# Kernel tuning notes

Measured on AMD Instinct MI355X. Metric: run time of the kernel, lower is better.

The kernel has to match this reference:

```python
import jax, jax.numpy as jnp
import numpy as np

B, N, F, H, OUT = 64, 512, 128, 256, 6


def setup_inputs() -> dict:
    key = jax.random.key(0)
    ks = jax.random.split(key, 20)
    s = 0.02
    inp = {
        "x": jax.random.normal(ks[0], (B * N, F), dtype=jnp.float32),
        "edge_index": jax.random.randint(ks[1], (2, 16), 0, B * N),
        "edge_weight": jax.random.uniform(ks[2], (16,), dtype=jnp.float32),
        "batch": jnp.repeat(jnp.arange(B, dtype=jnp.int64), N),
        "sigma": jax.random.uniform(ks[3], (1,), dtype=jnp.float32),
        "Wg": s * jax.random.normal(ks[4], (F, F)), "bg": jnp.zeros((F,)),
        "Wrel0": s * jax.random.normal(ks[5], (F, H)), "Wroot0": s * jax.random.normal(ks[6], (F, H)), "brel0": jnp.zeros((H,)),
        "Wrel1": s * jax.random.normal(ks[7], (H, H)), "Wroot1": s * jax.random.normal(ks[8], (H, H)), "brel1": jnp.zeros((H,)),
        "Wrel2": s * jax.random.normal(ks[9], (H, H)), "Wroot2": s * jax.random.normal(ks[10], (H, H)), "brel2": jnp.zeros((H,)),
        "W1": s * jax.random.normal(ks[11], (H, H)), "b1": jnp.zeros((H,)),
        "Wout": s * jax.random.normal(ks[12], (H, OUT)), "bout": jnp.zeros((OUT,)),
    }
    return inp


def _forward(x, sigma, Wg, bg, Wrel0, Wroot0, brel0, Wrel1, Wroot1, brel1,
             Wrel2, Wroot2, brel2, W1, b1, Wout, bout):
    # gdmLinear
    h = x @ Wg + bg                      # [B*N, F]
    hw = h.reshape(B, N, -1)             # to_dense_batch (equal-size windows)
    # pairwise squared distances per window -> Gaussian kernel
    sq = jnp.sum(hw * hw, axis=-1)       # [B, N]
    dist = jnp.maximum(sq[:, :, None] + sq[:, None, :]
                       - 2.0 * jnp.einsum('bnf,bmf->bnm', hw, hw), 0.0)
    A = jnp.exp(-dist / (2.0 * sigma[0] ** 2))   # [B, N, N], all > 0
    A = A * (1.0 - jnp.eye(N, dtype=A.dtype))    # nonzero extraction drops self-loops

    def conv(h, Wrel, Wroot, brel):
        # GraphConv: out_i = W_rel @ sum_j A[j,i] * h_j + b_rel + W_root @ h_i
        agg = jnp.einsum('bji,bjf->bif', A, h)
        return agg @ Wrel + brel + h @ Wroot

    h = hw
    h = jax.nn.relu(conv(h, Wrel0, Wroot0, brel0))
    h = jax.nn.relu(conv(h, Wrel1, Wroot1, brel1))
    h = conv(h, Wrel2, Wroot2, brel2)
    g = jnp.mean(h, axis=1)              # global_mean_pool (equal-size graphs)
    g = jax.nn.relu(g @ W1 + b1)
    return g @ Wout + bout               # [B, OUT]


def reference(x, edge_index, edge_weight, batch, sigma, Wg, bg,
              Wrel0, Wroot0, brel0, Wrel1, Wroot1, brel1,
              Wrel2, Wroot2, brel2, W1, b1, Wout, bout):
    # edge_index / edge_weight / batch inputs are recomputed internally by GdmGNN
    return _forward(x, sigma, Wg, bg, Wrel0, Wroot0, brel0, Wrel1, Wroot1, brel1,
                    Wrel2, Wroot2, brel2, W1, b1, Wout, bout)
```

## Files before the change

### kernel.cpp

```cpp
#include <hip/hip_runtime.h>
#include <math.h>

#define Bsz 64
#define Nn 512
#define Ff 128
#define Hh 256
#define OUTD 6
#define MTOT (Bsz * Nn)

typedef __bf16 bf16x8 __attribute__((ext_vector_type(8)));
typedef float f32x4 __attribute__((ext_vector_type(4)));
typedef int int4v __attribute__((ext_vector_type(4)));
typedef unsigned short ushort4v __attribute__((ext_vector_type(4)));

__device__ __forceinline__ unsigned short f2bf(float f) {
    unsigned u = __float_as_uint(f);
    u += 0x7FFFu + ((u >> 16) & 1u);
    return (unsigned short)(u >> 16);
}
__device__ __forceinline__ float bf2f(unsigned short s) {
    return __uint_as_float(((unsigned)s) << 16);
}

#define SWZ(r) (((r) ^ ((r) >> 2)) & 3)

__device__ __forceinline__ void async_ld16(const unsigned short* g, unsigned short* l) {
    __builtin_amdgcn_global_load_lds(
        (const __attribute__((address_space(1))) void*)g,
        (__attribute__((address_space(3))) void*)l,
        16, 0, 0);
}

__device__ __forceinline__ void wait_vm(int n) {
    switch (n) {
        case 0: asm volatile("s_waitcnt vmcnt(0)" ::: "memory"); break;
        case 1: asm volatile("s_waitcnt vmcnt(1)" ::: "memory"); break;
        case 2: asm volatile("s_waitcnt vmcnt(2)" ::: "memory"); break;
        case 3: asm volatile("s_waitcnt vmcnt(3)" ::: "memory"); break;
        case 4: asm volatile("s_waitcnt vmcnt(4)" ::: "memory"); break;
        case 5: asm volatile("s_waitcnt vmcnt(5)" ::: "memory"); break;
        default: asm volatile("s_waitcnt vmcnt(6)" ::: "memory"); break;
    }
}
__device__ __forceinline__ void pipe_barrier(int n) {
    wait_vm(n);
    __builtin_amdgcn_s_barrier();
    __builtin_amdgcn_sched_barrier(0);
}

#define LDH 40
#define TSZ (128 * 32)
#define ATS (256 * 32)
#define AGP 136
#define AGP1 264

__global__ __launch_bounds__(512) void fused_l0(
    const unsigned short* __restrict__ h0T,
    const unsigned short* __restrict__ Arows,
    const unsigned short* __restrict__ h0b,
    const unsigned short* __restrict__ WrelT0,
    const unsigned short* __restrict__ WrootT0,
    const float* __restrict__ brel0,
    unsigned short* __restrict__ h1b,
    unsigned short* __restrict__ h1T)
{
    int id = blockIdx.x;
    int b = id & 63;
    int nt = id >> 6;
    int n0g = nt * 128;
    long nodeBase = (long)b * Nn + n0g;

    const unsigned short* HT = h0T + (long)b * Ff * Nn;
    const unsigned short* AR = Arows + (long)b * Nn * Nn;

    __shared__ unsigned short SA[3 * ATS];
    __shared__ unsigned short SB[3 * TSZ];
    __shared__ unsigned short aggL[128 * AGP];

    int tid = threadIdx.x;
    int lane = tid & 63;
    int wave = tid >> 6;
    int quad = lane >> 4, l16 = lane & 15;
    int sr = lane >> 2, sc = lane & 3;

    {
        int wm = (wave >> 1) * 32, wn = (wave & 1) * 64;
        f32x4 acc[2][4] = {};
        auto issue = [&](int g) {
            int kk = g << 5;
            unsigned short* Ad = SA + (g % 3) * ATS;
            unsigned short* Bd = SB + (g % 3) * TSZ;
            int r = wave * 16 + sr;
            int c = sc ^ SWZ(r);
            async_ld16(HT + (long)r * Nn + kk + c * 8, Ad + (wave * 16) * 32);
            async_ld16(AR + (long)(n0g + r) * Nn + kk + c * 8, Bd + (wave * 16) * 32);
        };
        issue(0); issue(1);
        for (int g = 0; g < 16; ++g) {
            pipe_barrier(g + 1 < 16 ? 2 : 0);
            if (g + 2 < 16) issue(g + 2);
            const unsigned short* Ab = SA + (g % 3) * ATS;
            const unsigned short* Bb = SB + (g % 3) * TSZ;
            bf16x8 af[2], bfr[4];
            #pragma unroll
            for (int i = 0; i < 2; ++i) {
                int r = wm + i * 16 + l16;
                af[i] = *(const bf16x8*)&Ab[r * 32 + (quad ^ SWZ(r)) * 8];
            }
            #pragma unroll
            for (int j = 0; j < 4; ++j) {
                int r = wn + j * 16 + l16;
                bfr[j] = *(const bf16x8*)&Bb[r * 32 + (quad ^ SWZ(r)) * 8];
            }
            #pragma unroll
            for (int i = 0; i < 2; ++i)
                #pragma unroll
                for (int j = 0; j < 4; ++j)
                    acc[i][j] = __builtin_amdgcn_mfma_f32_16x16x32_bf16(
                        af[i], bfr[j], acc[i][j], 0, 0, 0);
        }
        #pragma unroll
        for (int i = 0; i < 2; ++i) {
            int f = wm + i * 16 + quad * 4;
            #pragma unroll
            for (int j = 0; j < 4; ++j) {
                int nl = wn + j * 16 + l16;
                f32x4 v = acc[i][j];
                ushort4v p;
                p[0] = f2bf(v[0]); p[1] = f2bf(v[1]);
                p[2] = f2bf(v[2]); p[3] = f2bf(v[3]);
                *(ushort4v*)&aggL[nl * AGP + f] = p;
            }
        }
    }
    __syncthreads();

    {
        int wm = (wave >> 1) * 64, wn = (wave & 1) * 64;
        f32x4 acc[4][4] = {};
        auto issue2 = [&](int g) {
            const unsigned short* Wp = (g < 4) ? WrelT0 : WrootT0;
            int kk = (g & 3) << 5;
            unsigned short* Ad = SA + (g % 3) * ATS;
            int r = wave * 16 + sr;
            int c = sc ^ SWZ(r);
            async_ld16(Wp + (long)r * Ff + kk + c * 8, Ad + (wave * 16) * 32);
            int r2 = 128 + r;
            int c2 = sc ^ SWZ(r2);
            async_ld16(Wp + (long)r2 * Ff + kk + c2 * 8, Ad + (128 + wave * 16) * 32);
            if (g >= 4) {
                unsigned short* Bd = SB + (g % 3) * TSZ;
                async_ld16(h0b + (nodeBase + r) * Ff + kk + c * 8,
                           Bd + (wave * 16) * 32);
            }
        };
        issue2(0); issue2(1);
        for (int g = 0; g < 8; ++g) {
            int nx = g + 1;
            pipe_barrier(nx >= 8 ? 0 : (nx < 4 ? 2 : 3));
            if (g + 2 < 8) issue2(g + 2);
            const unsigned short* Ab = SA + (g % 3) * ATS;
            bf16x8 af[4], bfr[4];
            #pragma unroll
            for (int i = 0; i < 4; ++i) {
                int r = wm + i * 16 + l16;
                af[i] = *(const bf16x8*)&Ab[r * 32 + (quad ^ SWZ(r)) * 8];
            }
            if (g < 4) {
                #pragma unroll
                for (int j = 0; j < 4; ++j) {
                    int nl = wn + j * 16 + l16;
                    bfr[j] = *(const bf16x8*)&aggL[nl * AGP + (g << 5) + quad * 8];
                }
            } else {
                const unsigned short* Bb = SB + (g % 3) * TSZ;
                #pragma unroll
                for (int j = 0; j < 4; ++j) {
                    int r = wn + j * 16 + l16;
                    bfr[j] = *(const bf16x8*)&Bb[r * 32 + (quad ^ SWZ(r)) * 8];
                }
            }
            #pragma unroll
            for (int i = 0; i < 4; ++i)
                #pragma unroll
                for (int j = 0; j < 4; ++j)
                    acc[i][j] = __builtin_amdgcn_mfma_f32_16x16x32_bf16(
                        af[i], bfr[j], acc[i][j], 0, 0, 0);
        }
        #pragma unroll
        for (int i = 0; i < 4; ++i) {
            int of = wm + i * 16 + quad * 4;
            float b0 = brel0[of + 0], b1 = brel0[of + 1];
            float b2 = brel0[of + 2], b3 = brel0[of + 3];
            #pragma unroll
            for (int j = 0; j < 4; ++j) {
                int nl = wn + j * 16 + l16;
                f32x4 v = acc[i][j];
                float o0 = fmaxf(v[0] + b0, 0.f), o1 = fmaxf(v[1] + b1, 0.f);
                float o2 = fmaxf(v[2] + b2, 0.f), o3 = fmaxf(v[3] + b3, 0.f);
                ushort4v p;
                p[0] = f2bf(o0); p[1] = f2bf(o1); p[2] = f2bf(o2); p[3] = f2bf(o3);
                *(ushort4v*)&h1b[(nodeBase + nl) * Hh + of] = p;
                long base = ((long)b * Hh) * 512 + n0g + nl;
                h1T[base + (long)(of + 0) * 512] = p[0];
                h1T[base + (long)(of + 1) * 512] = p[1];
                h1T[base + (long)(of + 2) * 512] = p[2];
                h1T[base + (long)(of + 3) * 512] = p[3];
            }
        }
    }
}

__global__ __launch_bounds__(512) void fused_l1(
    const unsigned short* __restrict__ h1T,
    const unsigned short* __restrict__ Arows,
    const unsigned short* __restrict__ h1b,
    const unsigned short* __restrict__ WrelT1,
    const unsigned short* __restrict__ WrootT1,
    const float* __restrict__ brel1,
    const float* __restrict__ w,
    float* __restrict__ vpart, float* __restrict__ mpart)
{
    constexpr int BTS = 128 * 32;

    int id = blockIdx.x;
    int b = id & 63;
    int nt = id >> 6;
    int n0g = nt * 128;
    long nodeBase = (long)b * Nn + n0g;

    const unsigned short* HT = h1T + (long)b * Hh * Nn;
    const unsigned short* AR = Arows + (long)b * Nn * Nn;

    __shared__ unsigned short SA[3 * ATS];
    __shared__ unsigned short SB[3 * BTS];
    __shared__ unsigned short aggL[128 * AGP1];

    int tid = threadIdx.x;
    int lane = tid & 63;
    int wave = tid >> 6;
    int quad = lane >> 4, l16 = lane & 15;
    int wm = (wave >> 1) * 64;
    int wn = (wave & 1) * 64;
    int sr = lane >> 2, sc = lane & 3;

    {
        f32x4 acc[4][4] = {};
        auto issue = [&](int g) {
            int kk = g << 5;
            unsigned short* Ad = SA + (g % 3) * ATS;
            int r = wave * 16 + sr;
            int c = sc ^ SWZ(r);
            async_ld16(HT + (long)r * Nn + kk + c * 8, Ad + (wave * 16) * 32);
            int r2 = 128 + r;
            int c2 = sc ^ SWZ(r2);
            async_ld16(HT + (long)r2 * Nn + kk + c2 * 8, Ad + (128 + wave * 16) * 32);
            unsigned short* Bd = SB + (g % 3) * BTS;
            async_ld16(AR + (long)(n0g + r) * Nn + kk + c * 8, Bd + (wave * 16) * 32);
        };
        issue(0); issue(1);
        for (int g = 0; g < 16; ++g) {
            pipe_barrier(g + 1 < 16 ? 3 : 0);
            if (g + 2 < 16) issue(g + 2);
            const unsigned short* Ab = SA + (g % 3) * ATS;
            const unsigned short* Bb = SB + (g % 3) * BTS;
            bf16x8 af[4], bfr[4];
            #pragma unroll
            for (int i = 0; i < 4; ++i) {
                int r = wm + i * 16 + l16;
                af[i] = *(const bf16x8*)&Ab[r * 32 + (quad ^ SWZ(r)) * 8];
            }
            #pragma unroll
            for (int j = 0; j < 4; ++j) {
                int r = wn + j * 16 + l16;
                bfr[j] = *(const bf16x8*)&Bb[r * 32 + (quad ^ SWZ(r)) * 8];
            }
            #pragma unroll
            for (int i = 0; i < 4; ++i)
                #pragma unroll
                for (int j = 0; j < 4; ++j)
                    acc[i][j] = __builtin_amdgcn_mfma_f32_16x16x32_bf16(
                        af[i], bfr[j], acc[i][j], 0, 0, 0);
        }
        #pragma unroll
        for (int i = 0; i < 4; ++i) {
            int f = wm + i * 16 + quad * 4;
            #pragma unroll
            for (int j = 0; j < 4; ++j) {
                int nl = wn + j * 16 + l16;
                f32x4 v = acc[i][j];
                ushort4v p;
                p[0] = f2bf(v[0]); p[1] = f2bf(v[1]);
                p[2] = f2bf(v[2]); p[3] = f2bf(v[3]);
                *(ushort4v*)&aggL[nl * AGP1 + f] = p;
            }
        }
    }
    __syncthreads();

    f32x4 acc[4][4] = {};
    auto issue2 = [&](int g) {
        const unsigned short* Wp = (g < 8) ? WrelT1 : WrootT1;
        int kk = (g & 7) << 5;
        unsigned short* Ad = SA + (g % 3) * ATS;
        int r = wave * 16 + sr;
        int c = sc ^ SWZ(r);
        async_ld16(Wp + (long)r * Hh + kk + c * 8, Ad + (wave * 16) * 32);
        int r2 = 128 + r;
        int c2 = sc ^ SWZ(r2);
        async_ld16(Wp + (long)r2 * Hh + kk + c2 * 8, Ad + (128 + wave * 16) * 32);
        if (g >= 8) {
            unsigned short* Bd = SB + (g % 3) * BTS;
            async_ld16(h1b + (nodeBase + r) * Hh + kk + c * 8, Bd + (wave * 16) * 32);
        }
    };
    issue2(0); issue2(1);
    for (int g = 0; g < 16; ++g) {
        int nx = g + 1;
        pipe_barrier(nx >= 16 ? 0 : (nx < 8 ? 2 : 3));
        if (g + 2 < 16) issue2(g + 2);
        const unsigned short* Ab = SA + (g % 3) * ATS;
        bf16x8 af[4], bfr[4];
        #pragma unroll
        for (int i = 0; i < 4; ++i) {
            int r = wm + i * 16 + l16;
            af[i] = *(const bf16x8*)&Ab[r * 32 + (quad ^ SWZ(r)) * 8];
        }
        if (g < 8) {
            #pragma unroll
            for (int j = 0; j < 4; ++j) {
                int nl = wn + j * 16 + l16;
                bfr[j] = *(const bf16x8*)&aggL[nl * AGP1 + (g << 5) + quad * 8];
            }
        } else {
            const unsigned short* Bb = SB + (g % 3) * BTS;
            #pragma unroll
            for (int j = 0; j < 4; ++j) {
                int r = wn + j * 16 + l16;
                bfr[j] = *(const bf16x8*)&Bb[r * 32 + (quad ^ SWZ(r)) * 8];
            }
        }
        #pragma unroll
        for (int i = 0; i < 4; ++i)
            #pragma unroll
            for (int j = 0; j < 4; ++j)
                acc[i][j] = __builtin_amdgcn_mfma_f32_16x16x32_bf16(
                    af[i], bfr[j], acc[i][j], 0, 0, 0);
    }

    #pragma unroll
    for (int i = 0; i < 4; ++i) {
        int lf = wm + i * 16 + quad * 4;
        float b0 = brel1[lf + 0], b1 = brel1[lf + 1];
        float b2 = brel1[lf + 2], b3 = brel1[lf + 3];
        float vp0 = 0.f, vp1 = 0.f, vp2 = 0.f, vp3 = 0.f;
        float mp0 = 0.f, mp1 = 0.f, mp2 = 0.f, mp3 = 0.f;
        #pragma unroll
        for (int j = 0; j < 4; ++j) {
            long node = nodeBase + wn + j * 16 + l16;
            f32x4 v = acc[i][j];
            float o0 = fmaxf(v[0] + b0, 0.f), o1 = fmaxf(v[1] + b1, 0.f);
            float o2 = fmaxf(v[2] + b2, 0.f), o3 = fmaxf(v[3] + b3, 0.f);
            float h0v = bf2f(f2bf(o0)), h1v = bf2f(f2bf(o1));
            float h2v = bf2f(f2bf(o2)), h3v = bf2f(f2bf(o3));
            float wv = w[node];
            vp0 += wv * h0v; vp1 += wv * h1v; vp2 += wv * h2v; vp3 += wv * h3v;
            mp0 += h0v; mp1 += h1v; mp2 += h2v; mp3 += h3v;
        }
        #pragma unroll
        for (int m = 1; m < 16; m <<= 1) {
            vp0 += __shfl_xor(vp0, m); vp1 += __shfl_xor(vp1, m);
            vp2 += __shfl_xor(vp2, m); vp3 += __shfl_xor(vp3, m);
            mp0 += __shfl_xor(mp0, m); mp1 += __shfl_xor(mp1, m);
            mp2 += __shfl_xor(mp2, m); mp3 += __shfl_xor(mp3, m);
        }
        if (l16 == 0) {
            long o = ((long)(b * 8 + nt * 2 + (wave & 1))) * Hh + lf;
            float4 vv = {vp0, vp1, vp2, vp3};
            float4 mm = {mp0, mp1, mp2, mp3};
            *(float4*)&vpart[o] = vv;
            *(float4*)&mpart[o] = mm;
        }
    }
}

__global__ __launch_bounds__(256) void prep_h0(
    const float* __restrict__ x, const float* __restrict__ Wg,
    const float* __restrict__ bg,
    const float* __restrict__ Wrel0, const float* __restrict__ Wroot0,
    const float* __restrict__ Wrel1, const float* __restrict__ Wroot1,
    unsigned short* __restrict__ T0, unsigned short* __restrict__ T1,
    unsigned short* __restrict__ T2, unsigned short* __restrict__ T3,
    float* __restrict__ w,
    unsigned short* __restrict__ h0b, unsigned short* __restrict__ h0T,
    float* __restrict__ sqv)
{
    if (blockIdx.x < 896) {
        int idx = blockIdx.x * 256 + threadIdx.x;
        if (idx >= 196608) { w[idx - 196608] = 0.f; return; }
        const float* src; unsigned short* dst; int kin; int e;
        if      (idx <  32768) { src = Wrel0;  dst = T0; kin = 128; e = idx; }
        else if (idx <  65536) { src = Wroot0; dst = T1; kin = 128; e = idx - 32768; }
        else if (idx < 131072) { src = Wrel1;  dst = T2; kin = 256; e = idx - 65536; }
        else                   { src = Wroot1; dst = T3; kin = 256; e = idx - 131072; }
        int o = (kin == 128) ? (e >> 7) : (e >> 8);
        int i = e & (kin - 1);
        dst[e] = f2bf(src[(long)i * 256 + o]);
        return;
    }

    __shared__ unsigned short As[128 * LDH];
    __shared__ unsigned short Bs[128 * LDH];
    __shared__ float rsq[128];

    int tid = threadIdx.x;
    int lane = tid & 63;
    int wave = tid >> 6;
    int quad = lane >> 4, l16 = lane & 15;
    int wm = (wave >> 1) * 64, wn = (wave & 1) * 64;
    int m0 = (blockIdx.x - 896) * 128;

    f32x4 acc[4][4] = {};

    for (int k0 = 0; k0 < Ff; k0 += 32) {
        __syncthreads();
        #pragma unroll
        for (int l = 0; l < 2; ++l) {
            int idx = tid + l * 256;
            int r = idx >> 2, ch = idx & 3;
            const float* px = x + (long)(m0 + r) * Ff + k0 + ch * 8;
            float4 xa = *(const float4*)px;
            float4 xb = *(const float4*)(px + 4);
            ushort4v pa, pb;
            pa[0] = f2bf(xa.x); pa[1] = f2bf(xa.y); pa[2] = f2bf(xa.z); pa[3] = f2bf(xa.w);
            pb[0] = f2bf(xb.x); pb[1] = f2bf(xb.y); pb[2] = f2bf(xb.z); pb[3] = f2bf(xb.w);
            *(ushort4v*)&As[r * LDH + ch * 8] = pa;
            *(ushort4v*)&As[r * LDH + ch * 8 + 4] = pb;
            int kk = k0 + ch * 8;
            ushort4v qa, qb;
            #pragma unroll
            for (int u = 0; u < 4; ++u) qa[u] = f2bf(Wg[(long)(kk + u) * 128 + r]);
            #pragma unroll
            for (int u = 0; u < 4; ++u) qb[u] = f2bf(Wg[(long)(kk + 4 + u) * 128 + r]);
            *(ushort4v*)&Bs[r * LDH + ch * 8] = qa;
            *(ushort4v*)&Bs[r * LDH + ch * 8 + 4] = qb;
        }
        __syncthreads();
        bf16x8 af[4], bfr[4];
        #pragma unroll
        for (int i = 0; i < 4; ++i)
            af[i] = *(const bf16x8*)&As[(wm + i * 16 + l16) * LDH + quad * 8];
        #pragma unroll
        for (int j = 0; j < 4; ++j)
            bfr[j] = *(const bf16x8*)&Bs[(wn + j * 16 + l16) * LDH + quad * 8];
        #pragma unroll
        for (int i = 0; i < 4; ++i)
            #pragma unroll
            for (int j = 0; j < 4; ++j)
                acc[i][j] = __builtin_amdgcn_mfma_f32_16x16x32_bf16(
                    af[i], bfr[j], acc[i][j], 0, 0, 0);
    }

    if (tid < 128) rsq[tid] = 0.f;
    __syncthreads();

    #pragma unroll
    for (int i = 0; i < 4; ++i) {
        int lrow = wm + i * 16 + quad * 4;
        int mb = m0 + lrow;
        float rp0 = 0.f, rp1 = 0.f, rp2 = 0.f, rp3 = 0.f;
        #pragma unroll
        for (int j = 0; j < 4; ++j) {
            int n = wn + j * 16 + l16;
            f32x4 v = acc[i][j];
            float bv = bg[n];
            unsigned short s0 = f2bf(v[0] + bv), s1 = f2bf(v[1] + bv);
            unsigned short s2 = f2bf(v[2] + bv), s3 = f2bf(v[3] + bv);
            h0b[(long)(mb + 0) * Ff + n] = s0;
            h0b[(long)(mb + 1) * Ff + n] = s1;
            h0b[(long)(mb + 2) * Ff + n] = s2;
            h0b[(long)(mb + 3) * Ff + n] = s3;
            ushort4v p; p[0] = s0; p[1] = s1; p[2] = s2; p[3] = s3;
            long ti = ((long)(mb >> 9) * Ff + n) * 512 + (mb & 511);
            *(ushort4v*)&h0T[ti] = p;
            float f0 = bf2f(s0), f1 = bf2f(s1), f2 = bf2f(s2), f3 = bf2f(s3);
            rp0 += f0 * f0; rp1 += f1 * f1; rp2 += f2 * f2; rp3 += f3 * f3;
        }
        #pragma unroll
        for (int m = 1; m < 16; m <<= 1) {
            rp0 += __shfl_xor(rp0, m);
            rp1 += __shfl_xor(rp1, m);
            rp2 += __shfl_xor(rp2, m);
            rp3 += __shfl_xor(rp3, m);
        }
        if (l16 == 0) {
            atomicAdd(&rsq[lrow + 0], rp0);
            atomicAdd(&rsq[lrow + 1], rp1);
            atomicAdd(&rsq[lrow + 2], rp2);
            atomicAdd(&rsq[lrow + 3], rp3);
        }
    }
    __syncthreads();
    if (tid < 128) sqv[m0 + tid] = rsq[tid];
}

__global__ __launch_bounds__(512) void gram_A_mfma(
    const unsigned short* __restrict__ h0b, const float* __restrict__ sqv,
    const float* __restrict__ sigma, unsigned short* __restrict__ Aout,
    float* __restrict__ w)
{
    int id = blockIdx.x;
    int b = id & 63;
    int t = id >> 6;
    int i0 = (t & 3) * 128, j0 = (t >> 2) * 128;

    const unsigned short* H = h0b + (long)b * Nn * Ff;
    const float* SQ = sqv + (long)b * Nn;
    unsigned short* Ab = Aout + (long)b * Nn * Nn;

    __shared__ unsigned short Is[2 * TSZ];
    __shared__ unsigned short Js[2 * TSZ];
    __shared__ float rsum[128];

    int tid = threadIdx.x;
    int lane = tid & 63;
    int wave = tid >> 6;
    int quad = lane >> 4, l16 = lane & 15;
    int wm = (wave >> 1) * 32, wn = (wave & 1) * 64;

    int sr = lane >> 2, sc = lane & 3;

    f32x4 acc[2][4] = {};

    auto issue = [&](int g) {
        int kk = g << 5;
        unsigned short* Id = Is + (g & 1) * TSZ;
        unsigned short* Jd = Js + (g & 1) * TSZ;
        int r = wave * 16 + sr;
        int c = sc ^ SWZ(r);
        async_ld16(H + (long)(i0 + r) * Ff + kk + c * 8, Id + (wave * 16) * 32);
        async_ld16(H + (long)(j0 + r) * Ff + kk + c * 8, Jd + (wave * 16) * 32);
    };

    issue(0);
    for (int g = 0; g < (Ff >> 5); ++g) {
        __syncthreads();
        if (g + 1 < (Ff >> 5)) issue(g + 1);
        const unsigned short* Ib = Is + (g & 1) * TSZ;
        const unsigned short* Jb = Js + (g & 1) * TSZ;
        bf16x8 af[2], bfr[4];
        #pragma unroll
        for (int i = 0; i < 2; ++i) {
            int r = wm + i * 16 + l16;
            af[i] = *(const bf16x8*)&Ib[r * 32 + (quad ^ SWZ(r)) * 8];
        }
        #pragma unroll
        for (int j = 0; j < 4; ++j) {
            int r = wn + j * 16 + l16;
            bfr[j] = *(const bf16x8*)&Jb[r * 32 + (quad ^ SWZ(r)) * 8];
        }
        #pragma unroll
        for (int i = 0; i < 2; ++i)
            #pragma unroll
            for (int j = 0; j < 4; ++j)
                acc[i][j] = __builtin_amdgcn_mfma_f32_16x16x32_bf16(
                    af[i], bfr[j], acc[i][j], 0, 0, 0);
    }

    if (tid < 128) rsum[tid] = 0.f;
    __syncthreads();

    float s = sigma[0];
    float inv2s2 = 1.0f / (2.0f * s * s);
    #pragma unroll
    for (int i = 0; i < 2; ++i) {
        int lrow = wm + i * 16 + quad * 4;
        int rb = i0 + lrow;
        float rs0 = 0.f, rs1 = 0.f, rs2 = 0.f, rs3 = 0.f;
        #pragma unroll
        for (int j = 0; j < 4; ++j) {
            int c = j0 + wn + j * 16 + l16;
            float sqc = SQ[c];
            f32x4 v = acc[i][j];
            ushort4v pk;
            float av[4];
            #pragma unroll
            for (int r4 = 0; r4 < 4; ++r4) {
                int r = rb + r4;
                float d = fmaxf(SQ[r] + sqc - 2.0f * v[r4], 0.0f);
                unsigned short a = (r == c) ? (unsigned short)0
                                            : f2bf(__expf(-d * inv2s2));
                pk[r4] = a;
                av[r4] = bf2f(a);
            }
            *(ushort4v*)&Ab[(long)c * Nn + rb] = pk;
            rs0 += av[0]; rs1 += av[1]; rs2 += av[2]; rs3 += av[3];
        }
        #pragma unroll
        for (int m = 1; m < 16; m <<= 1) {
            rs0 += __shfl_xor(rs0, m);
            rs1 += __shfl_xor(rs1, m);
            rs2 += __shfl_xor(rs2, m);
            rs3 += __shfl_xor(rs3, m);
        }
        if (l16 == 0) {
            atomicAdd(&rsum[lrow + 0], rs0);
            atomicAdd(&rsum[lrow + 1], rs1);
            atomicAdd(&rsum[lrow + 2], rs2);
            atomicAdd(&rsum[lrow + 3], rs3);
        }
    }
    __syncthreads();
    if (tid < 128) atomicAdd(&w[(long)b * Nn + i0 + tid], rsum[tid]);
}

__global__ __launch_bounds__(256) void head_kernel(
    const float* __restrict__ vpart, const float* __restrict__ mpart,
    const float* __restrict__ Wrel2, const float* __restrict__ Wroot2,
    const float* __restrict__ brel2,
    const float* __restrict__ W1, const float* __restrict__ b1,
    const float* __restrict__ Wout, const float* __restrict__ bout,
    float* __restrict__ out)
{
    int b = blockIdx.x;
    int j = threadIdx.x;
    __shared__ float vs[Hh], ms[Hh], gs[Hh], g2[Hh];
    float vp = 0.f, mp = 0.f;
    #pragma unroll
    for (int p = 0; p < 8; ++p) {
        long o = ((long)(b * 8 + p)) * Hh + j;
        vp += vpart[o];
        mp += mpart[o];
    }
    vs[j] = vp * (1.0f / (float)Nn);
    ms[j] = mp * (1.0f / (float)Nn);
    __syncthreads();
    float s = brel2[j];
    for (int c = 0; c < Hh; ++c)
        s += vs[c] * Wrel2[c * Hh + j] + ms[c] * Wroot2[c * Hh + j];
    gs[j] = s;
    __syncthreads();
    float t = b1[j];
    for (int k = 0; k < Hh; ++k) t += gs[k] * W1[k * Hh + j];
    g2[j] = fmaxf(t, 0.f);
    __syncthreads();
    if (j < OUTD) {
        float s2 = bout[j];
        for (int k = 0; k < Hh; ++k) s2 += g2[k] * Wout[k * OUTD + j];
        out[b * OUTD + j] = s2;
    }
}

extern "C" void kernel_launch(void* const* d_in, const int* in_sizes, int n_in,
                              void* d_out, int out_size, void* d_ws, size_t ws_size,
                              hipStream_t stream) {
    const float* x      = (const float*)d_in[0];
    const float* sigma  = (const float*)d_in[4];
    const float* Wg     = (const float*)d_in[5];
    const float* bg     = (const float*)d_in[6];
    const float* Wrel0  = (const float*)d_in[7];
    const float* Wroot0 = (const float*)d_in[8];
    const float* brel0  = (const float*)d_in[9];
    const float* Wrel1  = (const float*)d_in[10];
    const float* Wroot1 = (const float*)d_in[11];
    const float* brel1  = (const float*)d_in[12];
    const float* Wrel2  = (const float*)d_in[13];
    const float* Wroot2 = (const float*)d_in[14];
    const float* brel2  = (const float*)d_in[15];
    const float* W1     = (const float*)d_in[16];
    const float* b1     = (const float*)d_in[17];
    const float* Wout   = (const float*)d_in[18];
    const float* bout   = (const float*)d_in[19];
    float* out = (float*)d_out;

    char* ws = (char*)d_ws;
    unsigned short* h0b  = (unsigned short*)(ws + 16777216);
    unsigned short* h0T  = (unsigned short*)(ws + 25165824);
    float*          sq   = (float*)(ws + 33554432);
    unsigned short* Aadj = (unsigned short*)(ws + 33685504);
    unsigned short* h1b  = (unsigned short*)(ws + 84017152);
    unsigned short* h1T  = (unsigned short*)(ws + 100794368);
    unsigned short* WrelT0  = (unsigned short*)(ws + 167903232);
    unsigned short* WrootT0 = (unsigned short*)(ws + 167968768);
    unsigned short* WrelT1  = (unsigned short*)(ws + 168034304);
    unsigned short* WrootT1 = (unsigned short*)(ws + 168165376);
    float*          w     = (float*)(ws + 168558592);
    float*          vpart = (float*)(ws + 168689664);
    float*          mpart = (float*)(ws + 169213952);

    prep_h0<<<1152, 256, 0, stream>>>(x, Wg, bg, Wrel0, Wroot0, Wrel1, Wroot1,
                                      WrelT0, WrootT0, WrelT1, WrootT1,
                                      w, h0b, h0T, sq);

    gram_A_mfma<<<dim3(16 * Bsz, 1, 1), 512, 0, stream>>>(h0b, sq, sigma, Aadj, w);

    fused_l0<<<dim3(4 * Bsz, 1, 1), 512, 0, stream>>>(
        h0T, Aadj, h0b, WrelT0, WrootT0, brel0, h1b, h1T);

    fused_l1<<<dim3(4 * Bsz, 1, 1), 512, 0, stream>>>(
        h1T, Aadj, h1b, WrelT1, WrootT1, brel1, w, vpart, mpart);

    head_kernel<<<Bsz, 256, 0, stream>>>(vpart, mpart, Wrel2, Wroot2, brel2,
                                         W1, b1, Wout, bout, out);
}
```

Measured before the change: 212.4 us.

## Exploit Gram matrix symmetry to compute only upper-triangular tiles

The Gaussian adjacency kernel now launches 10 tile-pairs per graph instead of 16, computing only the upper-triangular 128x128 blocks of the symmetric distance matrix. Each off-diagonal tile writes both its transposed layout directly and its mirror through an LDS-staged transpose, and accumulates row and column sums into the degree vector. This cuts MFMA and exp work by about a third, at the cost of extra LDS traffic and a second global store pass per tile.

```diff
diff --git a/kernel.cpp b/kernel.cpp
--- a/kernel.cpp
+++ b/kernel.cpp
@@ -10,7 +10,6 @@
 
 typedef __bf16 bf16x8 __attribute__((ext_vector_type(8)));
 typedef float f32x4 __attribute__((ext_vector_type(4)));
-typedef int int4v __attribute__((ext_vector_type(4)));
 typedef unsigned short ushort4v __attribute__((ext_vector_type(4)));
 
 __device__ __forceinline__ unsigned short f2bf(float f) {
@@ -53,6 +52,7 @@
 #define ATS (256 * 32)
 #define AGP 136
 #define AGP1 264
+#define ATP 132
 
 __global__ __launch_bounds__(512) void fused_l0(
     const unsigned short* __restrict__ h0T,
@@ -504,38 +504,46 @@
     if (tid < 128) sqv[m0 + tid] = rsq[tid];
 }
 
-__global__ __launch_bounds__(512) void gram_A_mfma(
+__global__ __launch_bounds__(512) void gram_A_sym(
     const unsigned short* __restrict__ h0b, const float* __restrict__ sqv,
     const float* __restrict__ sigma, unsigned short* __restrict__ Aout,
     float* __restrict__ w)
 {
     int id = blockIdx.x;
     int b = id & 63;
-    int t = id >> 6;
-    int i0 = (t & 3) * 128, j0 = (t >> 2) * 128;
+    int tp = id >> 6;
+    int ti, tj;
+    if      (tp < 4) { ti = 0; tj = tp; }
+    else if (tp < 7) { ti = 1; tj = tp - 3; }
+    else if (tp < 9) { ti = 2; tj = tp - 5; }
+    else             { ti = 3; tj = 3; }
+    int i0 = ti * 128, j0 = tj * 128;
+    bool offd = (ti != tj);
 
     const unsigned short* H = h0b + (long)b * Nn * Ff;
     const float* SQ = sqv + (long)b * Nn;
     unsigned short* Ab = Aout + (long)b * Nn * Nn;
 
-    __shared__ unsigned short Is[2 * TSZ];
-    __shared__ unsigned short Js[2 * TSZ];
-    __shared__ float rsum[128];
+    __shared__ unsigned short POOL[128 * ATP];
+    __shared__ float rsI[128];
+    __shared__ float rsJ[128];
 
     int tid = threadIdx.x;
     int lane = tid & 63;
     int wave = tid >> 6;
     int quad = lane >> 4, l16 = lane & 15;
     int wm = (wave >> 1) * 32, wn = (wave & 1) * 64;
-
     int sr = lane >> 2, sc = lane & 3;
+
+    unsigned short* Is = POOL;
+    unsigned short* Js = POOL + 8192;
 
     f32x4 acc[2][4] = {};
 
     auto issue = [&](int g) {
         int kk = g << 5;
-        unsigned short* Id = Is + (g & 1) * TSZ;
-        unsigned short* Jd = Js + (g & 1) * TSZ;
+        unsigned short* Id = Is + (g & 1) * 4096;
+        unsigned short* Jd = Js + (g & 1) * 4096;
         int r = wave * 16 + sr;
         int c = sc ^ SWZ(r);
         async_ld16(H + (long)(i0 + r) * Ff + kk + c * 8, Id + (wave * 16) * 32);
@@ -546,8 +554,8 @@
     for (int g = 0; g < (Ff >> 5); ++g) {
         __syncthreads();
         if (g + 1 < (Ff >> 5)) issue(g + 1);
-        const unsigned short* Ib = Is + (g & 1) * TSZ;
-        const unsigned short* Jb = Js + (g & 1) * TSZ;
+        const unsigned short* Ib = Is + (g & 1) * 4096;
+        const unsigned short* Jb = Js + (g & 1) * 4096;
         bf16x8 af[2], bfr[4];
         #pragma unroll
         for (int i = 0; i < 2; ++i) {
@@ -567,33 +575,44 @@
                     af[i], bfr[j], acc[i][j], 0, 0, 0);
     }
 
-    if (tid < 128) rsum[tid] = 0.f;
-    __syncthreads();
-
+    if (tid < 128) { rsI[tid] = 0.f; rsJ[tid] = 0.f; }
+    __syncthreads();
+
+    unsigned short* AT = POOL;
     float s = sigma[0];
     float inv2s2 = 1.0f / (2.0f * s * s);
+    float colsum0 = 0.f, colsum1 = 0.f, colsum2 = 0.f, colsum3 = 0.f;
+
     #pragma unroll
     for (int i = 0; i < 2; ++i) {
         int lrow = wm + i * 16 + quad * 4;
-        int rb = i0 + lrow;
+        int rbg = i0 + lrow;
         float rs0 = 0.f, rs1 = 0.f, rs2 = 0.f, rs3 = 0.f;
         #pragma unroll
         for (int j = 0; j < 4; ++j) {
-            int c = j0 + wn + j * 16 + l16;
+            int cl = wn + j * 16 + l16;
+            int c = j0 + cl;
             float sqc = SQ[c];
             f32x4 v = acc[i][j];
             ushort4v pk;
             float av[4];
             #pragma unroll
             for (int r4 = 0; r4 < 4; ++r4) {
-                int r = rb + r4;
+                int r = rbg + r4;
                 float d = fmaxf(SQ[r] + sqc - 2.0f * v[r4], 0.0f);
                 unsigned short a = (r == c) ? (unsigned short)0
                                             : f2bf(__expf(-d * inv2s2));
                 pk[r4] = a;
                 av[r4] = bf2f(a);
-            }
-            *(ushort4v*)&Ab[(long)c * Nn + rb] = pk;
+                AT[(lrow + r4) * ATP + cl] = a;
+            }
+            if (offd)
+                *(ushort4v*)&Ab[(long)c * Nn + rbg] = pk;
+            float cs = av[0] + av[1] + av[2] + av[3];
+            if (j == 0) colsum0 += cs;
+            else if (j == 1) colsum1 += cs;
+            else if (j == 2) colsum2 += cs;
+            else colsum3 += cs;
             rs0 += av[0]; rs1 += av[1]; rs2 += av[2]; rs3 += av[3];
         }
         #pragma unroll
@@ -604,14 +623,42 @@
             rs3 += __shfl_xor(rs3, m);
         }
         if (l16 == 0) {
-            atomicAdd(&rsum[lrow + 0], rs0);
-            atomicAdd(&rsum[lrow + 1], rs1);
-            atomicAdd(&rsum[lrow + 2], rs2);
-            atomicAdd(&rsum[lrow + 3], rs3);
-        }
-    }
-    __syncthreads();
-    if (tid < 128) atomicAdd(&w[(long)b * Nn + i0 + tid], rsum[tid]);
+            atomicAdd(&rsI[lrow + 0], rs0);
+            atomicAdd(&rsI[lrow + 1], rs1);
+            atomicAdd(&rsI[lrow + 2], rs2);
+            atomicAdd(&rsI[lrow + 3], rs3);
+        }
+    }
+
+    if (offd) {
+        #pragma unroll
+        for (int j = 0; j < 4; ++j) {
+            float cs = (j == 0) ? colsum0 : (j == 1) ? colsum1
+                     : (j == 2) ? colsum2 : colsum3;
+            cs += __shfl_xor(cs, 16);
+            cs += __shfl_xor(cs, 32);
+            if (lane < 16)
+                atomicAdd(&rsJ[wn + j * 16 + l16], cs);
+        }
+    }
+    __syncthreads();
+
+    {
+        int row0 = tid >> 4, part = tid & 15;
+        #pragma unroll
+        for (int rr = 0; rr < 4; ++rr) {
+            int row = row0 + rr * 32;
+            ushort4v u0 = *(const ushort4v*)&AT[row * ATP + part * 8];
+            ushort4v u1 = *(const ushort4v*)&AT[row * ATP + part * 8 + 4];
+            unsigned short* gp = &Ab[(long)(i0 + row) * Nn + j0 + part * 8];
+            *(ushort4v*)gp = u0;
+            *(ushort4v*)(gp + 4) = u1;
+        }
+    }
+    if (tid < 128) {
+        atomicAdd(&w[(long)b * Nn + i0 + tid], rsI[tid]);
+        if (offd) atomicAdd(&w[(long)b * Nn + j0 + tid], rsJ[tid]);
+    }
 }
 
 __global__ __launch_bounds__(256) void head_kernel(
@@ -692,7 +739,7 @@
                                       WrelT0, WrootT0, WrelT1, WrootT1,
                                       w, h0b, h0T, sq);
 
-    gram_A_mfma<<<dim3(16 * Bsz, 1, 1), 512, 0, stream>>>(h0b, sq, sigma, Aadj, w);
+    gram_A_sym<<<dim3(10 * Bsz, 1, 1), 512, 0, stream>>>(h0b, sq, sigma, Aadj, w);
 
     fused_l0<<<dim3(4 * Bsz, 1, 1), 512, 0, stream>>>(
         h0T, Aadj, h0b, WrelT0, WrootT0, brel0, h1b, h1T);
```

After: 208.5 us. About the same (-1.8%).

## Fuse Gaussian adjacency computation into layer-0 aggregation kernel

Applied to the files above, without the earlier changes.

Removes the separate gram_A_mfma kernel and computes the Gaussian adjacency tiles inside the layer-0 kernel, chunk by chunk. Each tile is fed directly from shared memory into the aggregation MFMA instead of being re-read from global memory. The tile is still written to global for layer 1, and per-node row sums are written directly rather than via global atomics. The aggregation buffers also switch to a swizzled K-tiled shared layout. In exchange, the fused kernel launches only 256 blocks with about 120KB of shared memory, which lowers parallelism for the Gram phase and serializes it with the aggregation.

```diff
diff --git a/kernel.cpp b/kernel.cpp
--- a/kernel.cpp
+++ b/kernel.cpp
@@ -6,11 +6,9 @@
 #define Ff 128
 #define Hh 256
 #define OUTD 6
-#define MTOT (Bsz * Nn)
 
 typedef __bf16 bf16x8 __attribute__((ext_vector_type(8)));
 typedef float f32x4 __attribute__((ext_vector_type(4)));
-typedef int int4v __attribute__((ext_vector_type(4)));
 typedef unsigned short ushort4v __attribute__((ext_vector_type(4)));
 
 __device__ __forceinline__ unsigned short f2bf(float f) {
@@ -47,20 +45,25 @@
     __builtin_amdgcn_s_barrier();
     __builtin_amdgcn_sched_barrier(0);
 }
+__device__ __forceinline__ void drain_barrier() { pipe_barrier(0); }
 
 #define LDH 40
 #define TSZ (128 * 32)
 #define ATS (256 * 32)
-#define AGP 136
-#define AGP1 264
-
-__global__ __launch_bounds__(512) void fused_l0(
+
+__device__ __forceinline__ int tsw_idx(int kt, int nl, int fo) {
+    return kt * 4096 + nl * 32 + ((((fo >> 3) & 3) ^ SWZ(nl)) << 3) + (fo & 7);
+}
+
+__global__ __launch_bounds__(512) void fused_l0_gram(
+    const unsigned short* __restrict__ h0b,
     const unsigned short* __restrict__ h0T,
-    const unsigned short* __restrict__ Arows,
-    const unsigned short* __restrict__ h0b,
     const unsigned short* __restrict__ WrelT0,
     const unsigned short* __restrict__ WrootT0,
     const float* __restrict__ brel0,
+    const float* __restrict__ sqv, const float* __restrict__ sigma,
+    unsigned short* __restrict__ Aadj,
+    float* __restrict__ w,
     unsigned short* __restrict__ h1b,
     unsigned short* __restrict__ h1T)
 {
@@ -71,11 +74,18 @@
     long nodeBase = (long)b * Nn + n0g;
 
     const unsigned short* HT = h0T + (long)b * Ff * Nn;
-    const unsigned short* AR = Arows + (long)b * Nn * Nn;
-
-    __shared__ unsigned short SA[3 * ATS];
-    __shared__ unsigned short SB[3 * TSZ];
-    __shared__ unsigned short aggL[128 * AGP];
+    const float* SQ = sqv + (long)b * Nn;
+    unsigned short* Ab = Aadj + (long)b * Nn * Nn;
+
+    __shared__ __align__(16) unsigned char SMEM[123392];
+    unsigned short* H0R = (unsigned short*)(SMEM);
+    unsigned short* H0C = (unsigned short*)(SMEM + 32768);
+    unsigned short* ACH = (unsigned short*)(SMEM + 65536);
+    unsigned short* SAh = (unsigned short*)(SMEM + 98304);
+    float* rsum = (float*)(SMEM + 122880);
+    unsigned short* AGK = (unsigned short*)(SMEM);
+    unsigned short* SA2 = (unsigned short*)(SMEM + 32768);
+    unsigned short* SB2 = (unsigned short*)(SMEM + 81920);
 
     int tid = threadIdx.x;
     int lane = tid & 63;
@@ -83,57 +93,152 @@
     int quad = lane >> 4, l16 = lane & 15;
     int sr = lane >> 2, sc = lane & 3;
 
-    {
-        int wm = (wave >> 1) * 32, wn = (wave & 1) * 64;
-        f32x4 acc[2][4] = {};
-        auto issue = [&](int g) {
-            int kk = g << 5;
-            unsigned short* Ad = SA + (g % 3) * ATS;
-            unsigned short* Bd = SB + (g % 3) * TSZ;
-            int r = wave * 16 + sr;
-            int c = sc ^ SWZ(r);
-            async_ld16(HT + (long)r * Nn + kk + c * 8, Ad + (wave * 16) * 32);
-            async_ld16(AR + (long)(n0g + r) * Nn + kk + c * 8, Bd + (wave * 16) * 32);
-        };
-        issue(0); issue(1);
-        for (int g = 0; g < 16; ++g) {
-            pipe_barrier(g + 1 < 16 ? 2 : 0);
-            if (g + 2 < 16) issue(g + 2);
-            const unsigned short* Ab = SA + (g % 3) * ATS;
-            const unsigned short* Bb = SB + (g % 3) * TSZ;
+    float sg = sigma[0];
+    float inv2s2 = 1.0f / (2.0f * sg * sg);
+
+    auto issueH0R = [&]() {
+        int r = wave * 16 + sr;
+        int c = sc ^ SWZ(r);
+        #pragma unroll
+        for (int kt = 0; kt < 4; ++kt)
+            async_ld16(h0b + (nodeBase + r) * Ff + kt * 32 + c * 8,
+                       H0R + kt * 4096 + (wave * 16) * 32);
+    };
+    auto issueH0C = [&](int kc) {
+        const unsigned short* src = h0b + ((long)b * Nn + kc * 128) * Ff;
+        int r = wave * 16 + sr;
+        int c = sc ^ SWZ(r);
+        #pragma unroll
+        for (int kt = 0; kt < 4; ++kt)
+            async_ld16(src + (long)r * Ff + kt * 32 + c * 8,
+                       H0C + kt * 4096 + (wave * 16) * 32);
+    };
+    auto issueHT = [&](int g) {
+        int r = wave * 16 + sr;
+        int c = sc ^ SWZ(r);
+        async_ld16(HT + (long)r * Nn + g * 32 + c * 8,
+                   SAh + (g % 3) * 4096 + (wave * 16) * 32);
+    };
+
+    int wmS = (wave >> 1) * 32, wnS = (wave & 1) * 64;
+    f32x4 accS1[2][4] = {};
+    int wmG = (wave >> 1) * 32, wnG = (wave & 1) * 64;
+
+    if (tid < 128) rsum[tid] = 0.f;
+    issueH0R();
+    issueH0C(0);
+    issueHT(0);
+
+    for (int kc = 0; kc < 4; ++kc) {
+        drain_barrier();
+
+        f32x4 gr[2][4] = {};
+        #pragma unroll
+        for (int ks = 0; ks < 4; ++ks) {
             bf16x8 af[2], bfr[4];
             #pragma unroll
             for (int i = 0; i < 2; ++i) {
-                int r = wm + i * 16 + l16;
-                af[i] = *(const bf16x8*)&Ab[r * 32 + (quad ^ SWZ(r)) * 8];
-            }
-            #pragma unroll
-            for (int j = 0; j < 4; ++j) {
-                int r = wn + j * 16 + l16;
-                bfr[j] = *(const bf16x8*)&Bb[r * 32 + (quad ^ SWZ(r)) * 8];
+                int r = wmG + i * 16 + l16;
+                af[i] = *(const bf16x8*)&H0C[ks * 4096 + r * 32 + (quad ^ SWZ(r)) * 8];
+            }
+            #pragma unroll
+            for (int j = 0; j < 4; ++j) {
+                int r = wnG + j * 16 + l16;
+                bfr[j] = *(const bf16x8*)&H0R[ks * 4096 + r * 32 + (quad ^ SWZ(r)) * 8];
             }
             #pragma unroll
             for (int i = 0; i < 2; ++i)
                 #pragma unroll
                 for (int j = 0; j < 4; ++j)
-                    acc[i][j] = __builtin_amdgcn_mfma_f32_16x16x32_bf16(
-                        af[i], bfr[j], acc[i][j], 0, 0, 0);
-        }
-        #pragma unroll
-        for (int i = 0; i < 2; ++i) {
-            int f = wm + i * 16 + quad * 4;
-            #pragma unroll
-            for (int j = 0; j < 4; ++j) {
-                int nl = wn + j * 16 + l16;
-                f32x4 v = acc[i][j];
-                ushort4v p;
-                p[0] = f2bf(v[0]); p[1] = f2bf(v[1]);
-                p[2] = f2bf(v[2]); p[3] = f2bf(v[3]);
-                *(ushort4v*)&aggL[nl * AGP + f] = p;
-            }
+                    gr[i][j] = __builtin_amdgcn_mfma_f32_16x16x32_bf16(
+                        af[i], bfr[j], gr[i][j], 0, 0, 0);
+        }
+
+        {
+            float ws0 = 0.f, ws1 = 0.f, ws2 = 0.f, ws3 = 0.f;
+            #pragma unroll
+            for (int i = 0; i < 2; ++i) {
+                int krow = wmG + i * 16 + quad * 4;
+                int ktl = krow >> 5, fol = krow & 31;
+                #pragma unroll
+                for (int j = 0; j < 4; ++j) {
+                    int n = wnG + j * 16 + l16;
+                    int nglob = n0g + n;
+                    float sqn = SQ[nglob];
+                    f32x4 v = gr[i][j];
+                    ushort4v pk;
+                    float asum = 0.f;
+                    #pragma unroll
+                    for (int r4 = 0; r4 < 4; ++r4) {
+                        int kglob = kc * 128 + krow + r4;
+                        float d = fmaxf(sqn + SQ[kglob] - 2.0f * v[r4], 0.0f);
+                        unsigned short a = (nglob == kglob) ? (unsigned short)0
+                                                            : f2bf(__expf(-d * inv2s2));
+                        pk[r4] = a;
+                        asum += bf2f(a);
+                    }
+                    *(ushort4v*)&ACH[ktl * 4096 + n * 32 +
+                                     ((((fol >> 3) ^ SWZ(n)) << 3) + (fol & 7))] = pk;
+                    *(ushort4v*)&Ab[(long)nglob * Nn + kc * 128 + krow] = pk;
+                    if (j == 0) ws0 += asum;
+                    else if (j == 1) ws1 += asum;
+                    else if (j == 2) ws2 += asum;
+                    else ws3 += asum;
+                }
+            }
+            #pragma unroll
+            for (int j = 0; j < 4; ++j) {
+                float cs = (j == 0) ? ws0 : (j == 1) ? ws1 : (j == 2) ? ws2 : ws3;
+                cs += __shfl_xor(cs, 16);
+                cs += __shfl_xor(cs, 32);
+                if (lane < 16)
+                    atomicAdd(&rsum[wnG + j * 16 + l16], cs);
+            }
+        }
+        __syncthreads();
+
+        for (int t = 0; t < 4; ++t) {
+            int g = kc * 4 + t;
+            if (t < 3) issueHT(g + 1);
+            else if (kc < 3) { issueH0C(kc + 1); issueHT(g + 1); }
+            pipe_barrier(t < 3 ? 1 : (kc < 3 ? 5 : 0));
+            const unsigned short* Abf = SAh + (g % 3) * 4096;
+            bf16x8 af[2], bfr[4];
+            #pragma unroll
+            for (int i = 0; i < 2; ++i) {
+                int r = wmS + i * 16 + l16;
+                af[i] = *(const bf16x8*)&Abf[r * 32 + (quad ^ SWZ(r)) * 8];
+            }
+            #pragma unroll
+            for (int j = 0; j < 4; ++j) {
+                int nl = wnS + j * 16 + l16;
+                bfr[j] = *(const bf16x8*)&ACH[tsw_idx(t, nl, quad * 8)];
+            }
+            #pragma unroll
+            for (int i = 0; i < 2; ++i)
+                #pragma unroll
+                for (int j = 0; j < 4; ++j)
+                    accS1[i][j] = __builtin_amdgcn_mfma_f32_16x16x32_bf16(
+                        af[i], bfr[j], accS1[i][j], 0, 0, 0);
+        }
+    }
+
+    #pragma unroll
+    for (int i = 0; i < 2; ++i) {
+        int f = wmS + i * 16 + quad * 4;
+        int kt = f >> 5, fo = f & 31;
+        #pragma unroll
+        for (int j = 0; j < 4; ++j) {
+            int nl = wnS + j * 16 + l16;
+            f32x4 v = accS1[i][j];
+            ushort4v p;
+            p[0] = f2bf(v[0]); p[1] = f2bf(v[1]);
+            p[2] = f2bf(v[2]); p[3] = f2bf(v[3]);
+            *(ushort4v*)&AGK[tsw_idx(kt, nl, fo)] = p;
         }
     }
     __syncthreads();
+    if (tid < 128) w[(long)b * Nn + n0g + tid] = rsum[tid];
 
     {
         int wm = (wave >> 1) * 64, wn = (wave & 1) * 64;
@@ -141,7 +246,7 @@
         auto issue2 = [&](int g) {
             const unsigned short* Wp = (g < 4) ? WrelT0 : WrootT0;
             int kk = (g & 3) << 5;
-            unsigned short* Ad = SA + (g % 3) * ATS;
+            unsigned short* Ad = SA2 + (g % 3) * ATS;
             int r = wave * 16 + sr;
             int c = sc ^ SWZ(r);
             async_ld16(Wp + (long)r * Ff + kk + c * 8, Ad + (wave * 16) * 32);
@@ -149,7 +254,7 @@
             int c2 = sc ^ SWZ(r2);
             async_ld16(Wp + (long)r2 * Ff + kk + c2 * 8, Ad + (128 + wave * 16) * 32);
             if (g >= 4) {
-                unsigned short* Bd = SB + (g % 3) * TSZ;
+                unsigned short* Bd = SB2 + (g % 3) * TSZ;
                 async_ld16(h0b + (nodeBase + r) * Ff + kk + c * 8,
                            Bd + (wave * 16) * 32);
             }
@@ -159,21 +264,21 @@
             int nx = g + 1;
             pipe_barrier(nx >= 8 ? 0 : (nx < 4 ? 2 : 3));
             if (g + 2 < 8) issue2(g + 2);
-            const unsigned short* Ab = SA + (g % 3) * ATS;
+            const unsigned short* Abf = SA2 + (g % 3) * ATS;
             bf16x8 af[4], bfr[4];
             #pragma unroll
             for (int i = 0; i < 4; ++i) {
                 int r = wm + i * 16 + l16;
-                af[i] = *(const bf16x8*)&Ab[r * 32 + (quad ^ SWZ(r)) * 8];
+                af[i] = *(const bf16x8*)&Abf[r * 32 + (quad ^ SWZ(r)) * 8];
             }
             if (g < 4) {
                 #pragma unroll
                 for (int j = 0; j < 4; ++j) {
                     int nl = wn + j * 16 + l16;
-                    bfr[j] = *(const bf16x8*)&aggL[nl * AGP + (g << 5) + quad * 8];
+                    bfr[j] = *(const bf16x8*)&AGK[tsw_idx(g, nl, quad * 8)];
                 }
             } else {
-                const unsigned short* Bb = SB + (g % 3) * TSZ;
+                const unsigned short* Bb = SB2 + (g % 3) * TSZ;
                 #pragma unroll
                 for (int j = 0; j < 4; ++j) {
                     int r = wn + j * 16 + l16;
@@ -234,7 +339,7 @@
 
     __shared__ unsigned short SA[3 * ATS];
     __shared__ unsigned short SB[3 * BTS];
-    __shared__ unsigned short aggL[128 * AGP1];
+    __shared__ unsigned short AGK[8 * 128 * 32];
 
     int tid = threadIdx.x;
     int lane = tid & 63;
@@ -285,6 +390,7 @@
         #pragma unroll
         for (int i = 0; i < 4; ++i) {
             int f = wm + i * 16 + quad * 4;
+            int kt = f >> 5, fo = f & 31;
             #pragma unroll
             for (int j = 0; j < 4; ++j) {
                 int nl = wn + j * 16 + l16;
@@ -292,7 +398,7 @@
                 ushort4v p;
                 p[0] = f2bf(v[0]); p[1] = f2bf(v[1]);
                 p[2] = f2bf(v[2]); p[3] = f2bf(v[3]);
-                *(ushort4v*)&aggL[nl * AGP1 + f] = p;
+                *(ushort4v*)&AGK[tsw_idx(kt, nl, fo)] = p;
             }
         }
     }
@@ -330,7 +436,7 @@
             #pragma unroll
             for (int j = 0; j < 4; ++j) {
                 int nl = wn + j * 16 + l16;
-                bfr[j] = *(const bf16x8*)&aggL[nl * AGP1 + (g << 5) + quad * 8];
+                bfr[j] = *(const bf16x8*)&AGK[tsw_idx(g, nl, quad * 8)];
             }
         } else {
             const unsigned short* Bb = SB + (g % 3) * BTS;
@@ -504,116 +610,6 @@
     if (tid < 128) sqv[m0 + tid] = rsq[tid];
 }
 
-__global__ __launch_bounds__(512) void gram_A_mfma(
-    const unsigned short* __restrict__ h0b, const float* __restrict__ sqv,
-    const float* __restrict__ sigma, unsigned short* __restrict__ Aout,
-    float* __restrict__ w)
-{
-    int id = blockIdx.x;
-    int b = id & 63;
-    int t = id >> 6;
-    int i0 = (t & 3) * 128, j0 = (t >> 2) * 128;
-
-    const unsigned short* H = h0b + (long)b * Nn * Ff;
-    const float* SQ = sqv + (long)b * Nn;
-    unsigned short* Ab = Aout + (long)b * Nn * Nn;
-
-    __shared__ unsigned short Is[2 * TSZ];
-    __shared__ unsigned short Js[2 * TSZ];
-    __shared__ float rsum[128];
-
-    int tid = threadIdx.x;
-    int lane = tid & 63;
-    int wave = tid >> 6;
-    int quad = lane >> 4, l16 = lane & 15;
-    int wm = (wave >> 1) * 32, wn = (wave & 1) * 64;
-
-    int sr = lane >> 2, sc = lane & 3;
-
-    f32x4 acc[2][4] = {};
-
-    auto issue = [&](int g) {
-        int kk = g << 5;
-        unsigned short* Id = Is + (g & 1) * TSZ;
-        unsigned short* Jd = Js + (g & 1) * TSZ;
-        int r = wave * 16 + sr;
-        int c = sc ^ SWZ(r);
-        async_ld16(H + (long)(i0 + r) * Ff + kk + c * 8, Id + (wave * 16) * 32);
-        async_ld16(H + (long)(j0 + r) * Ff + kk + c * 8, Jd + (wave * 16) * 32);
-    };
-
-    issue(0);
-    for (int g = 0; g < (Ff >> 5); ++g) {
-        __syncthreads();
-        if (g + 1 < (Ff >> 5)) issue(g + 1);
-        const unsigned short* Ib = Is + (g & 1) * TSZ;
-        const unsigned short* Jb = Js + (g & 1) * TSZ;
-        bf16x8 af[2], bfr[4];
-        #pragma unroll
-        for (int i = 0; i < 2; ++i) {
-            int r = wm + i * 16 + l16;
-            af[i] = *(const bf16x8*)&Ib[r * 32 + (quad ^ SWZ(r)) * 8];
-        }
-        #pragma unroll
-        for (int j = 0; j < 4; ++j) {
-            int r = wn + j * 16 + l16;
-            bfr[j] = *(const bf16x8*)&Jb[r * 32 + (quad ^ SWZ(r)) * 8];
-        }
-        #pragma unroll
-        for (int i = 0; i < 2; ++i)
-            #pragma unroll
-            for (int j = 0; j < 4; ++j)
-                acc[i][j] = __builtin_amdgcn_mfma_f32_16x16x32_bf16(
-                    af[i], bfr[j], acc[i][j], 0, 0, 0);
-    }
-
-    if (tid < 128) rsum[tid] = 0.f;
-    __syncthreads();
-
-    float s = sigma[0];
-    float inv2s2 = 1.0f / (2.0f * s * s);
-    #pragma unroll
-    for (int i = 0; i < 2; ++i) {
-        int lrow = wm + i * 16 + quad * 4;
-        int rb = i0 + lrow;
-        float rs0 = 0.f, rs1 = 0.f, rs2 = 0.f, rs3 = 0.f;
-        #pragma unroll
-        for (int j = 0; j < 4; ++j) {
-            int c = j0 + wn + j * 16 + l16;
-            float sqc = SQ[c];
-            f32x4 v = acc[i][j];
-            ushort4v pk;
-            float av[4];
-            #pragma unroll
-            for (int r4 = 0; r4 < 4; ++r4) {
-                int r = rb + r4;
-                float d = fmaxf(SQ[r] + sqc - 2.0f * v[r4], 0.0f);
-                unsigned short a = (r == c) ? (unsigned short)0
-                                            : f2bf(__expf(-d * inv2s2));
-                pk[r4] = a;
-                av[r4] = bf2f(a);
-            }
-            *(ushort4v*)&Ab[(long)c * Nn + rb] = pk;
-            rs0 += av[0]; rs1 += av[1]; rs2 += av[2]; rs3 += av[3];
-        }
-        #pragma unroll
-        for (int m = 1; m < 16; m <<= 1) {
-            rs0 += __shfl_xor(rs0, m);
-            rs1 += __shfl_xor(rs1, m);
-            rs2 += __shfl_xor(rs2, m);
-            rs3 += __shfl_xor(rs3, m);
-        }
-        if (l16 == 0) {
-            atomicAdd(&rsum[lrow + 0], rs0);
-            atomicAdd(&rsum[lrow + 1], rs1);
-            atomicAdd(&rsum[lrow + 2], rs2);
-            atomicAdd(&rsum[lrow + 3], rs3);
-        }
-    }
-    __syncthreads();
-    if (tid < 128) atomicAdd(&w[(long)b * Nn + i0 + tid], rsum[tid]);
-}
-
 __global__ __launch_bounds__(256) void head_kernel(
     const float* __restrict__ vpart, const float* __restrict__ mpart,
     const float* __restrict__ Wrel2, const float* __restrict__ Wroot2,
@@ -692,10 +688,8 @@
                                       WrelT0, WrootT0, WrelT1, WrootT1,
                                       w, h0b, h0T, sq);
 
-    gram_A_mfma<<<dim3(16 * Bsz, 1, 1), 512, 0, stream>>>(h0b, sq, sigma, Aadj, w);
-
-    fused_l0<<<dim3(4 * Bsz, 1, 1), 512, 0, stream>>>(
-        h0T, Aadj, h0b, WrelT0, WrootT0, brel0, h1b, h1T);
+    fused_l0_gram<<<dim3(4 * Bsz, 1, 1), 512, 0, stream>>>(
+        h0b, h0T, WrelT0, WrootT0, brel0, sq, sigma, Aadj, w, h1b, h1T);
 
     fused_l1<<<dim3(4 * Bsz, 1, 1), 512, 0, stream>>>(
         h1T, Aadj, h1b, WrelT1, WrootT1, brel1, w, vpart, mpart);
```

After: 206.7 us, median of 2. 2.7% less time.
